# Optimization experiments

Measured on AMD Instinct MI355X. Metric: run time of the kernel, lower is better.

## Reference

```python
import jax, jax.numpy as jnp
import numpy as np
from jax import lax

EPS = 1e-5
K = 7
G = 4


def _dwconv_bn(x, w, g, b, m, v):
    # depthwise 3x3, pad 1, then BN (eval mode with running stats)
    C = x.shape[1]
    y = lax.conv_general_dilated(x, w, (1, 1), [(1, 1), (1, 1)],
                                 feature_group_count=C,
                                 dimension_numbers=('NCHW', 'OIHW', 'NCHW'))
    scale = (g / jnp.sqrt(v + EPS))[None, :, None, None]
    return (y - m[None, :, None, None]) * scale + b[None, :, None, None]


def _proj(t, pw1, pb1, pw2, pb2):
    # 1x1 conv -> GELU(exact) -> 1x1 conv, on small spatial maps
    h = jnp.einsum('bchw,oc->bohw', t, pw1) + pb1[None, :, None, None]
    h = jax.nn.gelu(h, approximate=False)
    return jnp.einsum('bchw,oc->bohw', h, pw2) + pb2[None, :, None, None]


def setup_inputs() -> dict:
    key = jax.random.key(0)
    ks = jax.random.split(key, 17)
    B, C, H, W = 16, 256, 56, 56
    r = C // 4
    inp = {
        'x1': jax.random.normal(ks[0], (B, C, H, W), jnp.float32),
        'dw1_w': jax.random.normal(ks[1], (C, 1, 3, 3), jnp.float32) * 0.1,
        'dw1_g': jax.random.uniform(ks[2], (C,), jnp.float32, 0.5, 1.5),
        'dw1_b': jax.random.normal(ks[3], (C,), jnp.float32) * 0.1,
        'dw1_m': jax.random.normal(ks[4], (C,), jnp.float32) * 0.1,
        'dw1_v': jax.random.uniform(ks[5], (C,), jnp.float32, 0.5, 1.5),
        'dw2_w': jax.random.normal(ks[6], (C, 1, 3, 3), jnp.float32) * 0.1,
        'dw2_g': jax.random.uniform(ks[7], (C,), jnp.float32, 0.5, 1.5),
        'dw2_b': jax.random.normal(ks[8], (C,), jnp.float32) * 0.1,
        'dw2_m': jax.random.normal(ks[9], (C,), jnp.float32) * 0.1,
        'dw2_v': jax.random.uniform(ks[10], (C,), jnp.float32, 0.5, 1.5),
        'weight1': jax.random.normal(ks[11], (G, C, K, K), jnp.float32) * 0.02,
        'bias1': jax.random.normal(ks[12], (G, C), jnp.float32) * 0.02,
        'pw1': jax.random.normal(ks[13], (r, C), jnp.float32) * 0.05,
        'pb1': jax.random.normal(ks[14], (r,), jnp.float32) * 0.05,
        'pw2': jax.random.normal(ks[15], (C * G, r), jnp.float32) * 0.05,
        'pb2': jax.random.normal(ks[16], (C * G,), jnp.float32) * 0.05,
    }
    return inp


def reference(x1, dw1_w, dw1_g, dw1_b, dw1_m, dw1_v,
              dw2_w, dw2_g, dw2_b, dw2_m, dw2_v,
              weight1, bias1, pw1, pb1, pw2, pb2):
    B, C, H, W = x1.shape
    # gated fuse: relu6(dw1(x)) * dw2(x)
    a = jnp.clip(_dwconv_bn(x1, dw1_w, dw1_g, dw1_b, dw1_m, dw1_v), 0.0, 6.0)
    x_fuse = a * _dwconv_bn(x1, dw2_w, dw2_g, dw2_b, dw2_m, dw2_v)

    # adaptive avg pool to (K,K): H,W multiples of K -> uniform block means
    pooled = x_fuse.reshape(B, C, K, H // K, K, W // K).mean(axis=(3, 5))

    # dynamic kernel: proj -> softmax over groups -> weighted sum of weight1
    scale1 = _proj(pooled, pw1, pb1, pw2, pb2).reshape(B, G, C, K, K)
    scale1 = jax.nn.softmax(scale1, axis=1)
    w_dyn = jnp.sum(scale1 * weight1[None], axis=1)  # [B, C, K, K]

    # dynamic bias
    mean_x = x_fuse.mean(axis=(-2, -1), keepdims=True)  # [B, C, 1, 1]
    sb = _proj(mean_x, pw1, pb1, pw2, pb2).reshape(B, G, C)
    sb = jax.nn.softmax(sb, axis=1)
    b_dyn = jnp.sum(sb * bias1[None], axis=1)  # [B, C]

    # per-sample depthwise conv with dynamic weights
    pad = K // 2

    def per_sample(xi, wi):  # xi [C,H,W], wi [C,K,K]
        y = lax.conv_general_dilated(xi[None], wi[:, None], (1, 1),
                                     [(pad, pad), (pad, pad)],
                                     feature_group_count=C,
                                     dimension_numbers=('NCHW', 'OIHW', 'NCHW'))
        return y[0]

    out = jax.vmap(per_sample)(x_fuse, w_dyn)  # [B, C, H, W]
    return out + b_dyn[:, :, None, None]
```

## Files before the change

### kernel.cpp

```cpp
#include <hip/hip_runtime.h>
#include <math.h>

#define BATCH 16
#define CH 256
#define HW 56
#define NPIX (HW*HW)
#define KK 7

__global__ __launch_bounds__(256, 4) void k1_fuse(
    const float* __restrict__ x1,
    const float* __restrict__ dw1w, const float* __restrict__ g1, const float* __restrict__ b1,
    const float* __restrict__ m1, const float* __restrict__ v1,
    const float* __restrict__ dw2w, const float* __restrict__ g2, const float* __restrict__ b2,
    const float* __restrict__ m2, const float* __restrict__ v2,
    float* __restrict__ xf,
    float* __restrict__ pooled)
{
    const int bc = blockIdx.x;
    const int c  = bc & 255;
    const int t  = threadIdx.x;

    __shared__ float part[196];

    float w1[9], w2[9];
    #pragma unroll
    for (int k = 0; k < 9; k++) { w1[k] = dw1w[c*9+k]; w2[k] = dw2w[c*9+k]; }
    const float sc1 = g1[c] * rsqrtf(v1[c] + 1e-5f);
    const float be1 = b1[c] - m1[c] * sc1;
    const float sc2 = g2[c] * rsqrtf(v2[c] + 1e-5f);
    const float be2 = b2[c] - m2[c] * sc2;

    const int ty = t / 14, tx = t - ty * 14;
    const float* plane = x1 + (size_t)bc * NPIX;

    float res[4][4];
    if (t < 196) {
        const int oy = 4 * ty;
        float y1a[4][4], y2a[4][4];
        #pragma unroll
        for (int a = 0; a < 4; a++)
            #pragma unroll
            for (int e = 0; e < 4; e++) { y1a[a][e] = 0.f; y2a[a][e] = 0.f; }

        #pragma unroll
        for (int iy = 0; iy < 6; iy++) {
            const int r   = oy - 1 + iy;
            const bool rok = (r >= 0) && (r < 56);
            const int rc  = rok ? r : 0;
            float rb[12];
            #pragma unroll
            for (int k = 0; k < 3; k++) {
                const int cx  = tx - 1 + k;
                const bool cv = (cx >= 0) && (cx < 14);
                const int cc2 = cv ? cx : 0;
                const bool ok = rok && cv;
                float4 v = *(const float4*)(plane + rc*56 + 4*cc2);
                rb[4*k+0] = ok ? v.x : 0.f;
                rb[4*k+1] = ok ? v.y : 0.f;
                rb[4*k+2] = ok ? v.z : 0.f;
                rb[4*k+3] = ok ? v.w : 0.f;
            }
            #pragma unroll
            for (int tyy = 0; tyy < 4; tyy++) {
                const int ky = iy - tyy;
                if (ky >= 0 && ky < 3) {
                    #pragma unroll
                    for (int e = 0; e < 4; e++)
                        #pragma unroll
                        for (int dj = 0; dj < 3; dj++) {
                            float xv = rb[3 + e + dj];
                            y1a[tyy][e] += xv * w1[ky*3+dj];
                            y2a[tyy][e] += xv * w2[ky*3+dj];
                        }
                }
            }
        }
        float tile_sum = 0.f;
        #pragma unroll
        for (int tyy = 0; tyy < 4; tyy++)
            #pragma unroll
            for (int e = 0; e < 4; e++) {
                float y1 = y1a[tyy][e] * sc1 + be1;
                float y2 = y2a[tyy][e] * sc2 + be2;
                float a = fminf(fmaxf(y1, 0.f), 6.f);
                res[tyy][e] = a * y2;
                tile_sum += res[tyy][e];
            }
        part[t] = tile_sum;
    }
    __syncthreads();
    if (t < 49) {
        int ph = t / 7, pw = t - ph * 7;
        float s = part[(2*ph  )*14 + 2*pw] + part[(2*ph  )*14 + 2*pw + 1]
                + part[(2*ph+1)*14 + 2*pw] + part[(2*ph+1)*14 + 2*pw + 1];
        pooled[(size_t)bc * 49 + t] = s * (1.f/64.f);
    }
    if (t < 196) {
        float* op = xf + (size_t)bc * NPIX;
        #pragma unroll
        for (int tyy = 0; tyy < 4; tyy++) {
            float4 r4; r4.x=res[tyy][0]; r4.y=res[tyy][1]; r4.z=res[tyy][2]; r4.w=res[tyy][3];
            *(float4*)(op + (4*ty + tyy)*56 + 4*tx) = r4;
        }
    }
}

__global__ __launch_bounds__(256) void k2a(
    const float* __restrict__ pooled, const float* __restrict__ pw1,
    const float* __restrict__ pb1, float* __restrict__ h)
{
    const int b  = blockIdx.x;
    const int oc = blockIdx.y;
    const int t  = threadIdx.x;
    __shared__ float pl[256*50];

    const float* pp = pooled + (size_t)b * 256 * 49;
    for (int idx = t; idx < 256*49; idx += 256) {
        int cc = idx / 49, p = idx - cc * 49;
        pl[cc*50 + p] = pp[idx];
    }
    __syncthreads();
    {
        float s = 0.f;
        #pragma unroll
        for (int p = 0; p < 49; p++) s += pl[t*50 + p];
        pl[t*50 + 49] = s * (1.f/49.f);
    }
    __syncthreads();

    for (int idx = t; idx < 16*50; idx += 256) {
        int ol = idx / 50, p = idx - ol * 50;
        int o = oc * 16 + ol;
        const float* wrow = pw1 + o * 256;
        float acc = pb1[o];
        #pragma unroll 8
        for (int cc = 0; cc < 256; cc++) acc += wrow[cc] * pl[cc*50 + p];
        float gv = 0.5f * acc * (1.f + erff(acc * 0.70710678118654752f));
        h[((size_t)b * 50 + p) * 64 + o] = gv;
    }
}

__global__ __launch_bounds__(256) void k2b(
    const float* __restrict__ h, const float* __restrict__ pw2, const float* __restrict__ pb2,
    const float* __restrict__ weight1, const float* __restrict__ bias1,
    float* __restrict__ w_dyn, float* __restrict__ b_dyn)
{
    const int b   = blockIdx.x;
    const int cch = blockIdx.y;
    const int t   = threadIdx.x;
    const int c_base = cch * 16;

    __shared__ __attribute__((aligned(16))) float hl[50*64];
    __shared__ float sl[64*51];

    const float* hp = h + (size_t)b * 50 * 64;
    for (int i = t; i < 800; i += 256) ((float4*)hl)[i] = ((const float4*)hp)[i];

    const int row = t & 63;
    const int pb  = t >> 6;
    const int g   = row >> 4, cl = row & 15;
    const int o2  = (g << 8) + c_base + cl;

    float wreg[64];
    {
        const float4* w4 = (const float4*)(pw2 + (size_t)o2 * 64);
        #pragma unroll
        for (int r4 = 0; r4 < 16; r4++) {
            float4 v = w4[r4];
            wreg[4*r4] = v.x; wreg[4*r4+1] = v.y; wreg[4*r4+2] = v.z; wreg[4*r4+3] = v.w;
        }
    }
    const float bias2 = pb2[o2];
    __syncthreads();

    for (int p = pb; p < 50; p += 4) {
        const float4* hv = (const float4*)&hl[p*64];
        float acc = bias2;
        #pragma unroll
        for (int r4 = 0; r4 < 16; r4++) {
            float4 v = hv[r4];
            acc += wreg[4*r4]*v.x + wreg[4*r4+1]*v.y + wreg[4*r4+2]*v.z + wreg[4*r4+3]*v.w;
        }
        sl[row*51 + p] = acc;
    }
    __syncthreads();

    for (int idx = t; idx < 16*50; idx += 256) {
        int cl2 = idx / 50, p = idx - cl2 * 50;
        float s0 = sl[(cl2     )*51 + p];
        float s1 = sl[(16 + cl2)*51 + p];
        float s2 = sl[(32 + cl2)*51 + p];
        float s3 = sl[(48 + cl2)*51 + p];
        float mx = fmaxf(fmaxf(s0, s1), fmaxf(s2, s3));
        float e0 = expf(s0-mx), e1 = expf(s1-mx), e2 = expf(s2-mx), e3 = expf(s3-mx);
        float inv = 1.f / (e0+e1+e2+e3);
        e0 *= inv; e1 *= inv; e2 *= inv; e3 *= inv;
        int cc = c_base + cl2;
        if (p < 49) {
            float wv = e0*weight1[(0*256+cc)*49+p] + e1*weight1[(1*256+cc)*49+p]
                     + e2*weight1[(2*256+cc)*49+p] + e3*weight1[(3*256+cc)*49+p];
            w_dyn[((size_t)b*256 + cc)*49 + p] = wv;
        } else {
            b_dyn[b*256 + cc] = e0*bias1[cc] + e1*bias1[256+cc] + e2*bias1[512+cc] + e3*bias1[768+cc];
        }
    }
}

#define S3 68
__global__ __launch_bounds__(256) void k3_dyn(
    const float* __restrict__ xf,
    const float* __restrict__ w_dyn, const float* __restrict__ b_dyn,
    float* __restrict__ out)
{
    const int bc = blockIdx.x;
    const int t  = threadIdx.x;
    __shared__ __attribute__((aligned(16))) float halo[62*S3];

    const float4* pl4 = (const float4*)(xf + (size_t)bc * NPIX);
    float4 v[4];
    if (t < 196) {
        #pragma unroll
        for (int q = 0; q < 4; q++) v[q] = pl4[q*196 + t];
    }

    {
        float4 z = make_float4(0.f, 0.f, 0.f, 0.f);
        float4* h4 = (float4*)halo;
        for (int i = t; i < 62*S3/4; i += 256) h4[i] = z;
    }

    float w[49];
    const float* wp = w_dyn + (size_t)bc * 49;
    #pragma unroll
    for (int k = 0; k < 49; k++) w[k] = wp[k];
    const float bias = b_dyn[bc];
    __syncthreads();

    if (t < 196) {
        #pragma unroll
        for (int q = 0; q < 4; q++) {
            int p = (q*196 + t) * 4;
            int i = p / 56, j = p - i * 56;
            *(float4*)&halo[(i+3)*S3 + 4 + j] = v[q];
        }
    }
    __syncthreads();

    if (t < 196) {
        const int ty = t / 14, tx = t - ty * 14;
        const int oy = ty * 4, ox = tx * 4;
        float acc[4][4];
        #pragma unroll
        for (int a = 0; a < 4; a++)
            #pragma unroll
            for (int bb = 0; bb < 4; bb++) acc[a][bb] = bias;

        #pragma unroll
        for (int iy = 0; iy < 10; iy++) {
            const float* hr = &halo[(oy+iy)*S3 + ox];
            float4 a = *(const float4*)hr;
            float4 b = *(const float4*)(hr + 4);
            float4 c = *(const float4*)(hr + 8);
            float row[12];
            row[0]=a.x; row[1]=a.y; row[2]=a.z; row[3]=a.w;
            row[4]=b.x; row[5]=b.y; row[6]=b.z; row[7]=b.w;
            row[8]=c.x; row[9]=c.y; row[10]=c.z; row[11]=c.w;
            #pragma unroll
            for (int tyy = 0; tyy < 4; tyy++) {
                const int ky = iy - tyy;
                if (ky >= 0 && ky < 7) {
                    #pragma unroll
                    for (int txx = 0; txx < 4; txx++)
                        #pragma unroll
                        for (int kx = 0; kx < 7; kx++)
                            acc[tyy][txx] += row[1+txx+kx] * w[ky*7+kx];
                }
            }
        }
        float* op = out + (size_t)bc * NPIX;
        #pragma unroll
        for (int tyy = 0; tyy < 4; tyy++) {
            float4 r4; r4.x = acc[tyy][0]; r4.y = acc[tyy][1]; r4.z = acc[tyy][2]; r4.w = acc[tyy][3];
            *(float4*)(op + (oy+tyy)*56 + ox) = r4;
        }
    }
}

extern "C" void kernel_launch(void* const* d_in, const int* in_sizes, int n_in,
                              void* d_out, int out_size, void* d_ws, size_t ws_size,
                              hipStream_t stream) {
    const float* x1    = (const float*)d_in[0];
    const float* dw1w  = (const float*)d_in[1];
    const float* dw1g  = (const float*)d_in[2];
    const float* dw1b  = (const float*)d_in[3];
    const float* dw1m  = (const float*)d_in[4];
    const float* dw1v  = (const float*)d_in[5];
    const float* dw2w  = (const float*)d_in[6];
    const float* dw2g  = (const float*)d_in[7];
    const float* dw2b  = (const float*)d_in[8];
    const float* dw2m  = (const float*)d_in[9];
    const float* dw2v  = (const float*)d_in[10];
    const float* weight1 = (const float*)d_in[11];
    const float* bias1   = (const float*)d_in[12];
    const float* pw1     = (const float*)d_in[13];
    const float* pb1     = (const float*)d_in[14];
    const float* pw2     = (const float*)d_in[15];
    const float* pb2     = (const float*)d_in[16];

    float* out = (float*)d_out;
    float* ws  = (float*)d_ws;
    float* xfuse  = ws;
    float* pooled = ws + 12845056;
    float* h      = ws + 13045760;
    float* w_dyn  = ws + 13096960;
    float* b_dyn  = ws + 13297664;

    k1_fuse<<<BATCH*CH, 256, 0, stream>>>(x1, dw1w, dw1g, dw1b, dw1m, dw1v,
                                          dw2w, dw2g, dw2b, dw2m, dw2v, xfuse, pooled);
    k2a<<<dim3(BATCH, 4), 256, 0, stream>>>(pooled, pw1, pb1, h);
    k2b<<<dim3(BATCH, 16), 256, 0, stream>>>(h, pw2, pb2, weight1, bias1, w_dyn, b_dyn);
    k3_dyn<<<BATCH*CH, 256, 0, stream>>>(xfuse, w_dyn, b_dyn, out);
}
```

Baseline: 215.9 us.

## Recompute fused depthwise stage in dynamic conv instead of storing intermediate

The first kernel now only computes the pooled means and no longer writes the full fused activation to workspace. The dynamic 7x7 conv kernel recomputes the two 3x3 depthwise convs, BN and gating directly from x1 into its shared-memory halo. This removes a full-tensor write and read (about 51 MB of global traffic) in exchange for doing the small 3x3 compute twice and putting more register pressure on k3. The launch-bounds occupancy hint of 4 on the first kernel is also dropped.

```diff
diff --git a/kernel.cpp b/kernel.cpp
--- a/kernel.cpp
+++ b/kernel.cpp
@@ -5,15 +5,70 @@
 #define CH 256
 #define HW 56
 #define NPIX (HW*HW)
-#define KK 7
-
-__global__ __launch_bounds__(256, 4) void k1_fuse(
+
+__device__ __forceinline__ void fuse_tile(
+    const float* __restrict__ plane, int ty, int tx,
+    const float w1[9], const float w2[9],
+    float sc1, float be1, float sc2, float be2,
+    float res[4][4])
+{
+    const int oy = 4 * ty;
+    float y1a[4][4], y2a[4][4];
+    #pragma unroll
+    for (int a = 0; a < 4; a++)
+        #pragma unroll
+        for (int e = 0; e < 4; e++) { y1a[a][e] = 0.f; y2a[a][e] = 0.f; }
+
+    #pragma unroll
+    for (int iy = 0; iy < 6; iy++) {
+        const int r    = oy - 1 + iy;
+        const bool rok = (r >= 0) && (r < 56);
+        const int rc   = rok ? r : 0;
+        float rb[12];
+        #pragma unroll
+        for (int k = 0; k < 3; k++) {
+            const int cx  = tx - 1 + k;
+            const bool cv = (cx >= 0) && (cx < 14);
+            const int cc2 = cv ? cx : 0;
+            const bool ok = rok && cv;
+            float4 v = *(const float4*)(plane + rc*56 + 4*cc2);
+            rb[4*k+0] = ok ? v.x : 0.f;
+            rb[4*k+1] = ok ? v.y : 0.f;
+            rb[4*k+2] = ok ? v.z : 0.f;
+            rb[4*k+3] = ok ? v.w : 0.f;
+        }
+        #pragma unroll
+        for (int tyy = 0; tyy < 4; tyy++) {
+            const int ky = iy - tyy;
+            if (ky >= 0 && ky < 3) {
+                #pragma unroll
+                for (int e = 0; e < 4; e++)
+                    #pragma unroll
+                    for (int dj = 0; dj < 3; dj++) {
+                        float xv = rb[3 + e + dj];
+                        y1a[tyy][e] += xv * w1[ky*3+dj];
+                        y2a[tyy][e] += xv * w2[ky*3+dj];
+                    }
+            }
+        }
+    }
+    #pragma unroll
+    for (int tyy = 0; tyy < 4; tyy++)
+        #pragma unroll
+        for (int e = 0; e < 4; e++) {
+            float y1 = y1a[tyy][e] * sc1 + be1;
+            float y2 = y2a[tyy][e] * sc2 + be2;
+            float a = fminf(fmaxf(y1, 0.f), 6.f);
+            res[tyy][e] = a * y2;
+        }
+}
+
+__global__ __launch_bounds__(256) void k1_pool(
     const float* __restrict__ x1,
     const float* __restrict__ dw1w, const float* __restrict__ g1, const float* __restrict__ b1,
     const float* __restrict__ m1, const float* __restrict__ v1,
     const float* __restrict__ dw2w, const float* __restrict__ g2, const float* __restrict__ b2,
     const float* __restrict__ m2, const float* __restrict__ v2,
-    float* __restrict__ xf,
     float* __restrict__ pooled)
 {
     const int bc = blockIdx.x;
@@ -30,63 +85,16 @@
     const float sc2 = g2[c] * rsqrtf(v2[c] + 1e-5f);
     const float be2 = b2[c] - m2[c] * sc2;
 
-    const int ty = t / 14, tx = t - ty * 14;
-    const float* plane = x1 + (size_t)bc * NPIX;
-
-    float res[4][4];
     if (t < 196) {
-        const int oy = 4 * ty;
-        float y1a[4][4], y2a[4][4];
+        const int ty = t / 14, tx = t - ty * 14;
+        float res[4][4];
+        fuse_tile(x1 + (size_t)bc * NPIX, ty, tx, w1, w2, sc1, be1, sc2, be2, res);
+        float s = 0.f;
         #pragma unroll
         for (int a = 0; a < 4; a++)
             #pragma unroll
-            for (int e = 0; e < 4; e++) { y1a[a][e] = 0.f; y2a[a][e] = 0.f; }
-
-        #pragma unroll
-        for (int iy = 0; iy < 6; iy++) {
-            const int r   = oy - 1 + iy;
-            const bool rok = (r >= 0) && (r < 56);
-            const int rc  = rok ? r : 0;
-            float rb[12];
-            #pragma unroll
-            for (int k = 0; k < 3; k++) {
-                const int cx  = tx - 1 + k;
-                const bool cv = (cx >= 0) && (cx < 14);
-                const int cc2 = cv ? cx : 0;
-                const bool ok = rok && cv;
-                float4 v = *(const float4*)(plane + rc*56 + 4*cc2);
-                rb[4*k+0] = ok ? v.x : 0.f;
-                rb[4*k+1] = ok ? v.y : 0.f;
-                rb[4*k+2] = ok ? v.z : 0.f;
-                rb[4*k+3] = ok ? v.w : 0.f;
-            }
-            #pragma unroll
-            for (int tyy = 0; tyy < 4; tyy++) {
-                const int ky = iy - tyy;
-                if (ky >= 0 && ky < 3) {
-                    #pragma unroll
-                    for (int e = 0; e < 4; e++)
-                        #pragma unroll
-                        for (int dj = 0; dj < 3; dj++) {
-                            float xv = rb[3 + e + dj];
-                            y1a[tyy][e] += xv * w1[ky*3+dj];
-                            y2a[tyy][e] += xv * w2[ky*3+dj];
-                        }
-                }
-            }
-        }
-        float tile_sum = 0.f;
-        #pragma unroll
-        for (int tyy = 0; tyy < 4; tyy++)
-            #pragma unroll
-            for (int e = 0; e < 4; e++) {
-                float y1 = y1a[tyy][e] * sc1 + be1;
-                float y2 = y2a[tyy][e] * sc2 + be2;
-                float a = fminf(fmaxf(y1, 0.f), 6.f);
-                res[tyy][e] = a * y2;
-                tile_sum += res[tyy][e];
-            }
-        part[t] = tile_sum;
+            for (int e = 0; e < 4; e++) s += res[a][e];
+        part[t] = s;
     }
     __syncthreads();
     if (t < 49) {
@@ -94,14 +102,6 @@
         float s = part[(2*ph  )*14 + 2*pw] + part[(2*ph  )*14 + 2*pw + 1]
                 + part[(2*ph+1)*14 + 2*pw] + part[(2*ph+1)*14 + 2*pw + 1];
         pooled[(size_t)bc * 49 + t] = s * (1.f/64.f);
-    }
-    if (t < 196) {
-        float* op = xf + (size_t)bc * NPIX;
-        #pragma unroll
-        for (int tyy = 0; tyy < 4; tyy++) {
-            float4 r4; r4.x=res[tyy][0]; r4.y=res[tyy][1]; r4.z=res[tyy][2]; r4.w=res[tyy][3];
-            *(float4*)(op + (4*ty + tyy)*56 + 4*tx) = r4;
-        }
     }
 }
 
@@ -208,46 +208,52 @@
 
 #define S3 68
 __global__ __launch_bounds__(256) void k3_dyn(
-    const float* __restrict__ xf,
+    const float* __restrict__ x1,
+    const float* __restrict__ dw1w, const float* __restrict__ g1, const float* __restrict__ b1,
+    const float* __restrict__ m1, const float* __restrict__ v1,
+    const float* __restrict__ dw2w, const float* __restrict__ g2, const float* __restrict__ b2,
+    const float* __restrict__ m2, const float* __restrict__ v2,
     const float* __restrict__ w_dyn, const float* __restrict__ b_dyn,
     float* __restrict__ out)
 {
     const int bc = blockIdx.x;
+    const int c  = bc & 255;
     const int t  = threadIdx.x;
     __shared__ __attribute__((aligned(16))) float halo[62*S3];
 
-    const float4* pl4 = (const float4*)(xf + (size_t)bc * NPIX);
-    float4 v[4];
-    if (t < 196) {
-        #pragma unroll
-        for (int q = 0; q < 4; q++) v[q] = pl4[q*196 + t];
-    }
+    float w1[9], w2[9];
+    #pragma unroll
+    for (int k = 0; k < 9; k++) { w1[k] = dw1w[c*9+k]; w2[k] = dw2w[c*9+k]; }
+    const float sc1 = g1[c] * rsqrtf(v1[c] + 1e-5f);
+    const float be1 = b1[c] - m1[c] * sc1;
+    const float sc2 = g2[c] * rsqrtf(v2[c] + 1e-5f);
+    const float be2 = b2[c] - m2[c] * sc2;
+    float wk[49];
+    const float* wp = w_dyn + (size_t)bc * 49;
+    #pragma unroll
+    for (int k = 0; k < 49; k++) wk[k] = wp[k];
+    const float bias = b_dyn[bc];
 
     {
         float4 z = make_float4(0.f, 0.f, 0.f, 0.f);
         float4* h4 = (float4*)halo;
         for (int i = t; i < 62*S3/4; i += 256) h4[i] = z;
     }
-
-    float w[49];
-    const float* wp = w_dyn + (size_t)bc * 49;
-    #pragma unroll
-    for (int k = 0; k < 49; k++) w[k] = wp[k];
-    const float bias = b_dyn[bc];
-    __syncthreads();
-
+    __syncthreads();
+
+    const int ty = t / 14, tx = t - ty * 14;
     if (t < 196) {
-        #pragma unroll
-        for (int q = 0; q < 4; q++) {
-            int p = (q*196 + t) * 4;
-            int i = p / 56, j = p - i * 56;
-            *(float4*)&halo[(i+3)*S3 + 4 + j] = v[q];
+        float res[4][4];
+        fuse_tile(x1 + (size_t)bc * NPIX, ty, tx, w1, w2, sc1, be1, sc2, be2, res);
+        #pragma unroll
+        for (int tyy = 0; tyy < 4; tyy++) {
+            float4 r4; r4.x=res[tyy][0]; r4.y=res[tyy][1]; r4.z=res[tyy][2]; r4.w=res[tyy][3];
+            *(float4*)&halo[(4*ty + tyy + 3)*S3 + 4 + 4*tx] = r4;
         }
     }
     __syncthreads();
 
     if (t < 196) {
-        const int ty = t / 14, tx = t - ty * 14;
         const int oy = ty * 4, ox = tx * 4;
         float acc[4][4];
         #pragma unroll
@@ -260,11 +266,11 @@
             const float* hr = &halo[(oy+iy)*S3 + ox];
             float4 a = *(const float4*)hr;
             float4 b = *(const float4*)(hr + 4);
-            float4 c = *(const float4*)(hr + 8);
+            float4 cc = *(const float4*)(hr + 8);
             float row[12];
             row[0]=a.x; row[1]=a.y; row[2]=a.z; row[3]=a.w;
             row[4]=b.x; row[5]=b.y; row[6]=b.z; row[7]=b.w;
-            row[8]=c.x; row[9]=c.y; row[10]=c.z; row[11]=c.w;
+            row[8]=cc.x; row[9]=cc.y; row[10]=cc.z; row[11]=cc.w;
             #pragma unroll
             for (int tyy = 0; tyy < 4; tyy++) {
                 const int ky = iy - tyy;
@@ -273,7 +279,7 @@
                     for (int txx = 0; txx < 4; txx++)
                         #pragma unroll
                         for (int kx = 0; kx < 7; kx++)
-                            acc[tyy][txx] += row[1+txx+kx] * w[ky*7+kx];
+                            acc[tyy][txx] += row[1+txx+kx] * wk[ky*7+kx];
                 }
             }
         }
@@ -309,15 +315,16 @@
 
     float* out = (float*)d_out;
     float* ws  = (float*)d_ws;
-    float* xfuse  = ws;
-    float* pooled = ws + 12845056;
-    float* h      = ws + 13045760;
-    float* w_dyn  = ws + 13096960;
-    float* b_dyn  = ws + 13297664;
-
-    k1_fuse<<<BATCH*CH, 256, 0, stream>>>(x1, dw1w, dw1g, dw1b, dw1m, dw1v,
-                                          dw2w, dw2g, dw2b, dw2m, dw2v, xfuse, pooled);
+    float* pooled = ws;
+    float* h      = ws + 200704;
+    float* w_dyn  = ws + 251904;
+    float* b_dyn  = ws + 452608;
+
+    k1_pool<<<BATCH*CH, 256, 0, stream>>>(x1, dw1w, dw1g, dw1b, dw1m, dw1v,
+                                          dw2w, dw2g, dw2b, dw2m, dw2v, pooled);
     k2a<<<dim3(BATCH, 4), 256, 0, stream>>>(pooled, pw1, pb1, h);
     k2b<<<dim3(BATCH, 16), 256, 0, stream>>>(h, pw2, pb2, weight1, bias1, w_dyn, b_dyn);
-    k3_dyn<<<BATCH*CH, 256, 0, stream>>>(xfuse, w_dyn, b_dyn, out);
-}
+    k3_dyn<<<BATCH*CH, 256, 0, stream>>>(x1, dw1w, dw1g, dw1b, dw1m, dw1v,
+                                         dw2w, dw2g, dw2b, dw2m, dw2v,
+                                         w_dyn, b_dyn, out);
+}
```

Result: faster. 202.1 us (-6.4%).
